# Kernel tuning notes

Hardware: AMD Instinct MI355X
Metric: run time of the kernel (lower is better)

The kernel has to match this reference:

```python
import jax, jax.numpy as jnp
import numpy as np

NUM_WORDS = 256  # max word index + 1 (sentinel row NUM_WORDS used to drop non-first-occurrence scatters)


def setup_inputs() -> dict:
    key = jax.random.key(0)
    ks = jax.random.split(key, 8)
    B, S, H, R, D, C = 16, 512, 768, 8, 512, 27
    hidden_states = jax.random.normal(ks[0], (B, S, H), jnp.float32)
    word_ids = jnp.sort(jax.random.randint(ks[1], (B, S), 0, NUM_WORDS), axis=-1)
    relations_positions = jax.random.randint(ks[2], (B, R), 0, S)
    w_rel = jax.random.normal(ks[3], (H,), jnp.float32) / np.sqrt(H).astype(np.float32)
    b_rel = jnp.zeros((1,), jnp.float32)
    w1 = jax.random.normal(ks[4], (2 * H, D), jnp.float32) / np.sqrt(2 * H).astype(np.float32)
    b1 = jnp.zeros((D,), jnp.float32)
    w2 = jax.random.normal(ks[5], (D, C), jnp.float32) / np.sqrt(D).astype(np.float32)
    b2 = jnp.zeros((C,), jnp.float32)
    return dict(hidden_states=hidden_states, word_ids=word_ids,
                relations_positions=relations_positions,
                w_rel=w_rel, b_rel=b_rel, w1=w1, b1=b1, w2=w2, b2=b2)


def reference(hidden_states, word_ids, relations_positions, w_rel, b_rel, w1, b1, w2, b2):
    B, S, H = hidden_states.shape
    # relational logits: Linear(H, 1).squeeze(-1)  -> [B, S]
    rel_logits = jnp.einsum('bsh,h->bs', hidden_states, w_rel) + b_rel

    # first_hidden_states[i, w] = hidden_states[i, j] at the FIRST token j of word w
    # (torch loop keys on word_id != prev_word_id; word_ids are monotone per row)
    first_occ = jnp.concatenate(
        [jnp.ones((B, 1), bool), word_ids[:, 1:] != word_ids[:, :-1]], axis=1)
    tgt = jnp.where(first_occ, word_ids, NUM_WORDS)  # route non-first tokens to sentinel row
    batch_idx = jnp.arange(B)[:, None]
    first_hidden = (jnp.zeros((B, NUM_WORDS + 1, H), hidden_states.dtype)
                    .at[batch_idx, tgt].set(hidden_states))[:, :NUM_WORDS]  # [B, W, H]

    # gather relation token embeddings -> [B, R, H]
    rel_hidden = jnp.take_along_axis(
        hidden_states, relations_positions[:, :, None], axis=1)

    # concat([word_embed, rel_embed]) @ w1 == word_embed @ w1[:H] + rel_embed @ w1[H:]
    h_word = jnp.einsum('bwh,hd->bwd', first_hidden, w1[:H])   # [B, W, D]
    h_rel = jnp.einsum('brh,hd->brd', rel_hidden, w1[H:])      # [B, R, D]
    hmid = jax.nn.relu(h_word[:, None, :, :] + h_rel[:, :, None, :] + b1)  # [B, R, W, D]
    role_logits = jnp.einsum('brwd,dc->brwc', hmid, w2) + b2   # [B, R, W, C]

    return rel_logits, role_logits
```

## Files before the change

### kernel.cpp

```cpp
#include <hip/hip_runtime.h>
#include <hip/hip_bf16.h>

#define BB 16
#define SS 512
#define HH 768
#define RR 8
#define DD 512
#define CC 27
#define WW 256

typedef __attribute__((ext_vector_type(8))) short short8;
typedef __attribute__((ext_vector_type(4))) float f32x4;

union PKu { unsigned short us[8]; uint4 u4; short8 s8; };

__device__ __forceinline__ unsigned short f32_to_bf16_rne(float v) {
    unsigned int u = __float_as_uint(v);
    unsigned int r = u + 0x7fffu + ((u >> 16) & 1u);
    return (unsigned short)(r >> 16);
}
__device__ __forceinline__ float bf16_to_f32(unsigned short u) {
    return __uint_as_float(((unsigned int)u) << 16);
}

__device__ __forceinline__ void glds16(const void* g, void* l) {
    __builtin_amdgcn_global_load_lds(
        (const __attribute__((address_space(1))) unsigned int*)g,
        (__attribute__((address_space(3))) unsigned int*)l, 16, 0, 0);
}


__global__ __launch_bounds__(256) void k_front(
    const float* __restrict__ hidden, const int* __restrict__ word_ids,
    const int* __restrict__ relpos, const float4* __restrict__ wrel4,
    const float* __restrict__ b_rel, const float* __restrict__ w1,
    const float* __restrict__ w2, float* __restrict__ out0,
    unsigned short* __restrict__ first_hidden,
    unsigned short* __restrict__ rel_hidden,
    unsigned short* __restrict__ w1t, unsigned short* __restrict__ w2t) {
    int bid = blockIdx.x, t = threadIdx.x;
    if (bid < 2048) {
        int lane = t & 63;
        int row = bid * 4 + (t >> 6);
        const float4* hid4 = (const float4*)hidden + (size_t)row * (HH / 4);
        float4 v[3];
        float acc = 0.f;
#pragma unroll
        for (int j = 0; j < 3; ++j) {
            v[j] = hid4[j * 64 + lane];
            float4 w = wrel4[j * 64 + lane];
            acc += v[j].x * w.x + v[j].y * w.y + v[j].z * w.z + v[j].w * w.w;
        }
#pragma unroll
        for (int off = 32; off > 0; off >>= 1) acc += __shfl_xor(acc, off, 64);
        if (lane == 0) out0[row] = acc + b_rel[0];
        int wid = word_ids[row];
        int s = row & (SS - 1);
        int prev = (s == 0) ? -1 : word_ids[row - 1];
        if (wid != prev) {
            int b = row >> 9;
            unsigned short* dst = first_hidden + (size_t)(b * WW + wid) * HH;
#pragma unroll
            for (int j = 0; j < 3; ++j) {
                union { unsigned short us[4]; uint2 u2; } pk;
                pk.us[0] = f32_to_bf16_rne(v[j].x);
                pk.us[1] = f32_to_bf16_rne(v[j].y);
                pk.us[2] = f32_to_bf16_rne(v[j].z);
                pk.us[3] = f32_to_bf16_rne(v[j].w);
                *(uint2*)(dst + j * 256 + lane * 4) = pk.u2;
            }
        }
        return;
    }
    int x = bid - 2048;
    if (x < 192) {
        __shared__ unsigned short tile[64][72];
        int kt = x >> 3, nt = x & 7;
        int i = t >> 2, j4 = (t & 3) * 16;
        const float* src = w1 + (size_t)(kt * 64 + i) * DD + nt * 64 + j4;
#pragma unroll
        for (int v = 0; v < 4; ++v) {
            float4 f = *(const float4*)(src + v * 4);
            tile[i][j4 + v * 4 + 0] = f32_to_bf16_rne(f.x);
            tile[i][j4 + v * 4 + 1] = f32_to_bf16_rne(f.y);
            tile[i][j4 + v * 4 + 2] = f32_to_bf16_rne(f.z);
            tile[i][j4 + v * 4 + 3] = f32_to_bf16_rne(f.w);
        }
        __syncthreads();
        int jj = t >> 2, cb = (t & 3) * 16;
        union { unsigned short us[16]; uint4 u4[2]; } ov;
#pragma unroll
        for (int v = 0; v < 16; ++v) ov.us[v] = tile[cb + v][jj];
        unsigned short* dst = w1t + (size_t)(nt * 64 + jj) * (2 * HH) + kt * 64 + cb;
        *(uint4*)(dst) = ov.u4[0];
        *(uint4*)(dst + 8) = ov.u4[1];
    } else if (x == 192) {
        for (int idx = t; idx < 32 * DD; idx += 256) {
            int n = idx >> 9, k = idx & (DD - 1);
            float v = (n < CC) ? w2[(size_t)k * CC + n] : 0.f;
            w2t[n * DD + k] = f32_to_bf16_rne(v);
        }
    } else {
        __shared__ int pres[WW];
        int b = x - 193;
        pres[t] = 0;
        __syncthreads();
        for (int s = t; s < SS; s += 256) pres[word_ids[b * SS + s]] = 1;
        __syncthreads();
        if (!pres[t]) {
            uint4 z = {0u, 0u, 0u, 0u};
            unsigned short* dst = first_hidden + (size_t)(b * WW + t) * HH;
#pragma unroll 4
            for (int c = 0; c < 96; ++c) *(uint4*)(dst + c * 8) = z;
        }
        for (int idx = t; idx < 1024; idx += 256) {
            int rr = idx >> 7, c = idx & 127;
            if (c < 96) {
                int pos = relpos[b * RR + rr];
                const float* srow = hidden + (size_t)(b * SS + pos) * HH + c * 8;
                PKu pk;
#pragma unroll
                for (int e = 0; e < 8; ++e) pk.us[e] = f32_to_bf16_rne(srow[e]);
                *(uint4*)(rel_hidden + (size_t)(b * RR + rr) * HH + c * 8) = pk.u4;
            }
        }
    }
}

__global__ __launch_bounds__(256) void k_gemm(
    const unsigned short* __restrict__ first_hidden,
    const unsigned short* __restrict__ rel_hidden,
    const unsigned short* __restrict__ w1t, const float* __restrict__ b1,
    unsigned short* __restrict__ h_word, unsigned short* __restrict__ h_rel) {
    __shared__ __align__(16) unsigned char a_s[32768];
    __shared__ __align__(16) unsigned char b_s[16384];
    int nt = blockIdx.x;
    int mt = blockIdx.y;
    bool isw = (mt < 32);
    const unsigned short* A = isw ? first_hidden : rel_hidden;
    unsigned short* C = isw ? h_word : h_rel;
    int kbase = isw ? 0 : HH;
    int m0 = isw ? mt * 128 : 0;
    int t = threadIdx.x;
    int wv = t >> 6, lane = t & 63;
    int wr = wv >> 1, wc = wv & 1;
    int q = lane >> 4, r = lane & 15;

    const unsigned char* aP[4];
    const unsigned char* bP[2];
    unsigned lofa[4], lofb[2];
#pragma unroll
    for (int j = 0; j < 4; ++j) {
        int ci = j * 256 + t;
        int row = ci >> 3, ch = ci & 7;
        int sc = ch ^ (row & 7);
        aP[j] = (const unsigned char*)A + (size_t)(m0 + row) * (HH * 2) + sc * 16;
        lofa[j] = ci * 16;
    }
#pragma unroll
    for (int j = 0; j < 2; ++j) {
        int ci = j * 256 + t;
        int row = ci >> 3, ch = ci & 7;
        int sc = ch ^ (row & 7);
        bP[j] = (const unsigned char*)w1t + (size_t)(nt * 64 + row) * (2 * HH * 2)
                + (size_t)kbase * 2 + sc * 16;
        lofb[j] = ci * 16;
    }
    int arow[4], brow[2];
#pragma unroll
    for (int mi = 0; mi < 4; ++mi) arow[mi] = wr * 64 + mi * 16 + r;
#pragma unroll
    for (int ni = 0; ni < 2; ++ni) brow[ni] = wc * 32 + ni * 16 + r;

    f32x4 acc[4][2];
#pragma unroll
    for (int mi = 0; mi < 4; ++mi)
#pragma unroll
        for (int ni = 0; ni < 2; ++ni) acc[mi][ni] = (f32x4){0.f, 0.f, 0.f, 0.f};

#pragma unroll
    for (int j = 0; j < 4; ++j) glds16(aP[j], a_s + lofa[j]);
#pragma unroll
    for (int j = 0; j < 2; ++j) glds16(bP[j], b_s + lofb[j]);
    __syncthreads();

    for (int kt = 0; kt < 12; ++kt) {
        if (kt < 11) {
            unsigned na = ((kt + 1) & 1) * 16384;
            unsigned nb = ((kt + 1) & 1) * 8192;
#pragma unroll
            for (int j = 0; j < 4; ++j) glds16(aP[j] + (kt + 1) * 128, a_s + na + lofa[j]);
#pragma unroll
            for (int j = 0; j < 2; ++j) glds16(bP[j] + (kt + 1) * 128, b_s + nb + lofb[j]);
        }
        unsigned ba = (kt & 1) * 16384;
        unsigned bb = (kt & 1) * 8192;
#pragma unroll
        for (int ks = 0; ks < 2; ++ks) {
            int c = ks * 4 + q;
            short8 bfr[2];
#pragma unroll
            for (int ni = 0; ni < 2; ++ni)
                bfr[ni] = *(const short8*)(b_s + bb + brow[ni] * 128 +
                            ((c ^ (brow[ni] & 7)) << 4));
#pragma unroll
            for (int mi = 0; mi < 4; ++mi) {
                short8 af = *(const short8*)(a_s + ba + arow[mi] * 128 +
                            ((c ^ (arow[mi] & 7)) << 4));
                acc[mi][0] = __builtin_amdgcn_mfma_f32_16x16x32_bf16(
                    af, bfr[0], acc[mi][0], 0, 0, 0);
                acc[mi][1] = __builtin_amdgcn_mfma_f32_16x16x32_bf16(
                    af, bfr[1], acc[mi][1], 0, 0, 0);
            }
        }
        __syncthreads();
    }
    float bias[2];
#pragma unroll
    for (int ni = 0; ni < 2; ++ni) {
        int n = nt * 64 + wc * 32 + ni * 16 + r;
        bias[ni] = isw ? b1[n] : 0.f;
    }
#pragma unroll
    for (int mi = 0; mi < 4; ++mi) {
        int m = m0 + wr * 64 + mi * 16 + q * 4;
#pragma unroll
        for (int ni = 0; ni < 2; ++ni) {
            int n = nt * 64 + wc * 32 + ni * 16 + r;
#pragma unroll
            for (int reg = 0; reg < 4; ++reg)
                C[(size_t)(m + reg) * DD + n] =
                    f32_to_bf16_rne(acc[mi][ni][reg] + bias[ni]);
        }
    }
}

__global__ __launch_bounds__(512) void k_role(
    const unsigned short* __restrict__ h_word, const unsigned short* __restrict__ h_rel,
    const unsigned short* __restrict__ w2t, const float* __restrict__ b2,
    float* __restrict__ out_role) {
    int wt = blockIdx.x;
    int b  = blockIdx.y;
    int t  = threadIdx.x;
    __shared__ __align__(16) unsigned char hw_s[16384];
    __shared__ float hr_s[RR][DD];
    __shared__ __align__(16) unsigned char w2_s[32768];
    int wv = t >> 6, lane = t & 63;
    {
#pragma unroll
        for (int i = 0; i < 2; ++i) {
            int row = wv * 2 + i;
            const unsigned short* src = h_word +
                (size_t)(b * WW + wt * 16 + row) * DD + ((lane ^ (row & 7)) * 8);
            glds16(src, hw_s + row * 1024 + lane * 16);
        }
    }
    {
#pragma unroll
        for (int i = 0; i < 4; ++i) {
            int row = wv * 4 + i;
            const unsigned short* src = w2t + row * DD + ((lane ^ (row & 7)) * 8);
            glds16(src, w2_s + row * 1024 + lane * 16);
        }
    }
    {
        int rr = t >> 6, c = t & 63;
        PKu hv;
        hv.u4 = *(const uint4*)(h_rel + (size_t)(b * RR + rr) * DD + c * 8);
        float4 o0, o1;
        o0.x = bf16_to_f32(hv.us[0]); o0.y = bf16_to_f32(hv.us[1]);
        o0.z = bf16_to_f32(hv.us[2]); o0.w = bf16_to_f32(hv.us[3]);
        o1.x = bf16_to_f32(hv.us[4]); o1.y = bf16_to_f32(hv.us[5]);
        o1.z = bf16_to_f32(hv.us[6]); o1.w = bf16_to_f32(hv.us[7]);
        *(float4*)&hr_s[rr][c * 8]     = o0;
        *(float4*)&hr_s[rr][c * 8 + 4] = o1;
    }
    __syncthreads();
    int q = lane >> 4, wl = lane & 15;
    int rr = wv;
    unsigned wlx = (wl & 7) << 4;
    f32x4 acc[2];
#pragma unroll
    for (int ni = 0; ni < 2; ++ni) acc[ni] = (f32x4){0.f, 0.f, 0.f, 0.f};

#pragma unroll 2
    for (int ks = 0; ks < DD / 32; ++ks) {
        int c = 4 * ks + q;
        short8 bfr[2];
#pragma unroll
        for (int ni = 0; ni < 2; ++ni) {
            int n = ni * 16 + wl;
            bfr[ni] = *(const short8*)(w2_s + n * 1024 + ((c ^ (n & 7)) << 4));
        }
        PKu hw;
        hw.u4 = *(const uint4*)(hw_s + wl * 1024 + ((unsigned)(c << 4) ^ wlx));
        const float* hrp = &hr_s[rr][ks * 32 + q * 8];
        float4 h0 = *(const float4*)(hrp);
        float4 h1 = *(const float4*)(hrp + 4);
        PKu pk;
        pk.us[0] = f32_to_bf16_rne(fmaxf(bf16_to_f32(hw.us[0]) + h0.x, 0.f));
        pk.us[1] = f32_to_bf16_rne(fmaxf(bf16_to_f32(hw.us[1]) + h0.y, 0.f));
        pk.us[2] = f32_to_bf16_rne(fmaxf(bf16_to_f32(hw.us[2]) + h0.z, 0.f));
        pk.us[3] = f32_to_bf16_rne(fmaxf(bf16_to_f32(hw.us[3]) + h0.w, 0.f));
        pk.us[4] = f32_to_bf16_rne(fmaxf(bf16_to_f32(hw.us[4]) + h1.x, 0.f));
        pk.us[5] = f32_to_bf16_rne(fmaxf(bf16_to_f32(hw.us[5]) + h1.y, 0.f));
        pk.us[6] = f32_to_bf16_rne(fmaxf(bf16_to_f32(hw.us[6]) + h1.z, 0.f));
        pk.us[7] = f32_to_bf16_rne(fmaxf(bf16_to_f32(hw.us[7]) + h1.w, 0.f));
#pragma unroll
        for (int ni = 0; ni < 2; ++ni)
            acc[ni] = __builtin_amdgcn_mfma_f32_16x16x32_bf16(
                pk.s8, bfr[ni], acc[ni], 0, 0, 0);
    }
#pragma unroll
    for (int ni = 0; ni < 2; ++ni) {
        int c = ni * 16 + wl;
        if (c < CC) {
#pragma unroll
            for (int reg = 0; reg < 4; ++reg) {
                int wg = wt * 16 + 4 * q + reg;
                out_role[(size_t)((b * RR + rr) * WW + wg) * CC + c] =
                    acc[ni][reg] + b2[c];
            }
        }
    }
}

extern "C" void kernel_launch(void* const* d_in, const int* in_sizes, int n_in,
                              void* d_out, int out_size, void* d_ws, size_t ws_size,
                              hipStream_t stream) {
    const float* hidden   = (const float*)d_in[0];
    const int*   word_ids = (const int*)d_in[1];
    const int*   relpos   = (const int*)d_in[2];
    const float* w_rel    = (const float*)d_in[3];
    const float* b_rel    = (const float*)d_in[4];
    const float* w1       = (const float*)d_in[5];
    const float* b1       = (const float*)d_in[6];
    const float* w2       = (const float*)d_in[7];
    const float* b2       = (const float*)d_in[8];

    float* out0 = (float*)d_out;
    float* out1 = out0 + BB * SS;

    unsigned short* first_hidden = (unsigned short*)d_ws;
    unsigned short* rel_hidden   = (unsigned short*)((char*)d_ws + 6291456);
    unsigned short* w1t          = (unsigned short*)((char*)d_ws + 6488064);
    unsigned short* w2t          = (unsigned short*)((char*)d_ws + 8060928);
    unsigned short* h_word       = (unsigned short*)((char*)d_ws + 8093696);
    unsigned short* h_rel        = (unsigned short*)((char*)d_ws + 12288000);

    k_front<<<2048 + 209, 256, 0, stream>>>(
        hidden, word_ids, relpos, (const float4*)w_rel, b_rel, w1, w2,
        out0, first_hidden, rel_hidden, w1t, w2t);
    k_gemm<<<dim3(8, 33), 256, 0, stream>>>(
        first_hidden, rel_hidden, w1t, b1, h_word, h_rel);
    k_role<<<dim3(WW / 16, BB), 512, 0, stream>>>(h_word, h_rel, w2t, b2, out1);
}
```

Before: 44.59 us.

## Halve GEMM M-tile to 64 and remap blocks XCD-aware on a 1D grid

Shrinks the k_gemm tile from 128x64 to 64x64, doubling the block count from 264 to 528 so the 256 CUs are filled more evenly. Block IDs now come from a 1D grid and are remapped so each XCD gets a group of M-tiles that share B tiles, aiming for better L2 locality. The cost is fewer MFMAs per LDS load and more redundant reads of w1t across the extra tiles. The k_role loading code is only restructured, with no change in behaviour.

```diff
diff --git a/kernel.cpp b/kernel.cpp
--- a/kernel.cpp
+++ b/kernel.cpp
@@ -132,80 +132,83 @@
     const unsigned short* __restrict__ rel_hidden,
     const unsigned short* __restrict__ w1t, const float* __restrict__ b1,
     unsigned short* __restrict__ h_word, unsigned short* __restrict__ h_rel) {
-    __shared__ __align__(16) unsigned char a_s[32768];
+    __shared__ __align__(16) unsigned char a_s[16384];
     __shared__ __align__(16) unsigned char b_s[16384];
-    int nt = blockIdx.x;
-    int mt = blockIdx.y;
-    bool isw = (mt < 32);
+    int bid = blockIdx.x;
+    int nt, m0;
+    bool isw;
+    if (bid < 512) {
+        int xcd = bid & 7, k = bid >> 3;
+        int mt = xcd + 8 * (k & 7);
+        nt = k >> 3;
+        isw = true;
+        m0 = mt * 64;
+    } else {
+        int jj = bid - 512;
+        isw = false;
+        m0 = (jj >> 3) * 64;
+        nt = jj & 7;
+    }
     const unsigned short* A = isw ? first_hidden : rel_hidden;
     unsigned short* C = isw ? h_word : h_rel;
     int kbase = isw ? 0 : HH;
-    int m0 = isw ? mt * 128 : 0;
     int t = threadIdx.x;
     int wv = t >> 6, lane = t & 63;
     int wr = wv >> 1, wc = wv & 1;
     int q = lane >> 4, r = lane & 15;
 
-    const unsigned char* aP[4];
+    const unsigned char* aP[2];
     const unsigned char* bP[2];
-    unsigned lofa[4], lofb[2];
-#pragma unroll
-    for (int j = 0; j < 4; ++j) {
-        int ci = j * 256 + t;
+    unsigned lofa[2], lofb[2];
+#pragma unroll
+    for (int g = 0; g < 2; ++g) {
+        int ci = g * 256 + t;
         int row = ci >> 3, ch = ci & 7;
         int sc = ch ^ (row & 7);
-        aP[j] = (const unsigned char*)A + (size_t)(m0 + row) * (HH * 2) + sc * 16;
-        lofa[j] = ci * 16;
-    }
-#pragma unroll
-    for (int j = 0; j < 2; ++j) {
-        int ci = j * 256 + t;
-        int row = ci >> 3, ch = ci & 7;
-        int sc = ch ^ (row & 7);
-        bP[j] = (const unsigned char*)w1t + (size_t)(nt * 64 + row) * (2 * HH * 2)
+        aP[g] = (const unsigned char*)A + (size_t)(m0 + row) * (HH * 2) + sc * 16;
+        lofa[g] = ci * 16;
+        bP[g] = (const unsigned char*)w1t + (size_t)(nt * 64 + row) * (2 * HH * 2)
                 + (size_t)kbase * 2 + sc * 16;
-        lofb[j] = ci * 16;
-    }
-    int arow[4], brow[2];
-#pragma unroll
-    for (int mi = 0; mi < 4; ++mi) arow[mi] = wr * 64 + mi * 16 + r;
+        lofb[g] = ci * 16;
+    }
+    int arow[2], brow[2];
+#pragma unroll
+    for (int mi = 0; mi < 2; ++mi) arow[mi] = wr * 32 + mi * 16 + r;
 #pragma unroll
     for (int ni = 0; ni < 2; ++ni) brow[ni] = wc * 32 + ni * 16 + r;
 
-    f32x4 acc[4][2];
-#pragma unroll
-    for (int mi = 0; mi < 4; ++mi)
+    f32x4 acc[2][2];
+#pragma unroll
+    for (int mi = 0; mi < 2; ++mi)
 #pragma unroll
         for (int ni = 0; ni < 2; ++ni) acc[mi][ni] = (f32x4){0.f, 0.f, 0.f, 0.f};
 
 #pragma unroll
-    for (int j = 0; j < 4; ++j) glds16(aP[j], a_s + lofa[j]);
-#pragma unroll
-    for (int j = 0; j < 2; ++j) glds16(bP[j], b_s + lofb[j]);
+    for (int g = 0; g < 2; ++g) glds16(aP[g], a_s + lofa[g]);
+#pragma unroll
+    for (int g = 0; g < 2; ++g) glds16(bP[g], b_s + lofb[g]);
     __syncthreads();
 
     for (int kt = 0; kt < 12; ++kt) {
         if (kt < 11) {
-            unsigned na = ((kt + 1) & 1) * 16384;
             unsigned nb = ((kt + 1) & 1) * 8192;
 #pragma unroll
-            for (int j = 0; j < 4; ++j) glds16(aP[j] + (kt + 1) * 128, a_s + na + lofa[j]);
-#pragma unroll
-            for (int j = 0; j < 2; ++j) glds16(bP[j] + (kt + 1) * 128, b_s + nb + lofb[j]);
-        }
-        unsigned ba = (kt & 1) * 16384;
-        unsigned bb = (kt & 1) * 8192;
+            for (int g = 0; g < 2; ++g) glds16(aP[g] + (kt + 1) * 128, a_s + nb + lofa[g]);
+#pragma unroll
+            for (int g = 0; g < 2; ++g) glds16(bP[g] + (kt + 1) * 128, b_s + nb + lofb[g]);
+        }
+        unsigned bo = (kt & 1) * 8192;
 #pragma unroll
         for (int ks = 0; ks < 2; ++ks) {
             int c = ks * 4 + q;
             short8 bfr[2];
 #pragma unroll
             for (int ni = 0; ni < 2; ++ni)
-                bfr[ni] = *(const short8*)(b_s + bb + brow[ni] * 128 +
+                bfr[ni] = *(const short8*)(b_s + bo + brow[ni] * 128 +
                             ((c ^ (brow[ni] & 7)) << 4));
 #pragma unroll
-            for (int mi = 0; mi < 4; ++mi) {
-                short8 af = *(const short8*)(a_s + ba + arow[mi] * 128 +
+            for (int mi = 0; mi < 2; ++mi) {
+                short8 af = *(const short8*)(a_s + bo + arow[mi] * 128 +
                             ((c ^ (arow[mi] & 7)) << 4));
                 acc[mi][0] = __builtin_amdgcn_mfma_f32_16x16x32_bf16(
                     af, bfr[0], acc[mi][0], 0, 0, 0);
@@ -222,8 +225,8 @@
         bias[ni] = isw ? b1[n] : 0.f;
     }
 #pragma unroll
-    for (int mi = 0; mi < 4; ++mi) {
-        int m = m0 + wr * 64 + mi * 16 + q * 4;
+    for (int mi = 0; mi < 2; ++mi) {
+        int m = m0 + wr * 32 + mi * 16 + q * 4;
 #pragma unroll
         for (int ni = 0; ni < 2; ++ni) {
             int n = nt * 64 + wc * 32 + ni * 16 + r;
@@ -246,25 +249,21 @@
     __shared__ float hr_s[RR][DD];
     __shared__ __align__(16) unsigned char w2_s[32768];
     int wv = t >> 6, lane = t & 63;
+#pragma unroll
+    for (int i = 0; i < 2; ++i) {
+        int row = wv * 2 + i;
+        const unsigned short* src = h_word +
+            (size_t)(b * WW + wt * 16 + row) * DD + ((lane ^ (row & 7)) * 8);
+        glds16(src, hw_s + row * 1024 + lane * 16);
+    }
+#pragma unroll
+    for (int i = 0; i < 4; ++i) {
+        int row = wv * 4 + i;
+        const unsigned short* src = w2t + row * DD + ((lane ^ (row & 7)) * 8);
+        glds16(src, w2_s + row * 1024 + lane * 16);
+    }
     {
-#pragma unroll
-        for (int i = 0; i < 2; ++i) {
-            int row = wv * 2 + i;
-            const unsigned short* src = h_word +
-                (size_t)(b * WW + wt * 16 + row) * DD + ((lane ^ (row & 7)) * 8);
-            glds16(src, hw_s + row * 1024 + lane * 16);
-        }
-    }
-    {
-#pragma unroll
-        for (int i = 0; i < 4; ++i) {
-            int row = wv * 4 + i;
-            const unsigned short* src = w2t + row * DD + ((lane ^ (row & 7)) * 8);
-            glds16(src, w2_s + row * 1024 + lane * 16);
-        }
-    }
-    {
-        int rr = t >> 6, c = t & 63;
+        int rr = wv, c = lane;
         PKu hv;
         hv.u4 = *(const uint4*)(h_rel + (size_t)(b * RR + rr) * DD + c * 8);
         float4 o0, o1;
@@ -351,7 +350,7 @@
     k_front<<<2048 + 209, 256, 0, stream>>>(
         hidden, word_ids, relpos, (const float4*)w_rel, b_rel, w1, w2,
         out0, first_hidden, rel_hidden, w1t, w2t);
-    k_gemm<<<dim3(8, 33), 256, 0, stream>>>(
+    k_gemm<<<528, 256, 0, stream>>>(
         first_hidden, rel_hidden, w1t, b1, h_word, h_rel);
     k_role<<<dim3(WW / 16, BB), 512, 0, stream>>>(h_word, h_rel, w2t, b2, out1);
 }
```

Result: faster. 40.14 us (-10.0%).
